# Kernel optimization log

Measured on AMD Instinct MI355X. Metric: run time of the kernel, lower is better.

## Reference

```python
import jax, jax.numpy as jnp
import numpy as np

B, T, Fd, C, D = 16, 256, 128, 32, 32
K_RATIO = 0.5
EPS = 1e-5


def setup_inputs() -> dict:
    key = jax.random.key(0)
    ks = jax.random.split(key, 40)
    n = lambda i, shape, s=0.05: jax.random.normal(ks[i], shape, jnp.float32) * s
    inp = {"x": jax.random.normal(ks[0], (B, T, Fd, C), jnp.float32)}
    inp.update(c1w=n(1, (C, C)), c1b=n(2, (C,)), bng=1.0 + n(3, (C,)), bnb=n(4, (C,)),
               bnm=n(5, (C,)), bnv=jax.random.uniform(ks[6], (C,)) + 0.5,
               c2w=n(7, (1, C)), c2b=n(8, (1,)))
    def gat_params(i0, pre):
        return {pre + "apw": n(i0, (D, C)), pre + "apb": n(i0 + 1, (D,)),
                pre + "aw": n(i0 + 2, (D,)), pre + "pww": n(i0 + 3, (D, C)),
                pre + "pwb": n(i0 + 4, (D,)), pre + "pow": n(i0 + 5, (D, C)),
                pre + "pob": n(i0 + 6, (D,)), pre + "g": 1.0 + n(i0 + 7, (D,)),
                pre + "be": n(i0 + 8, (D,)), pre + "m": n(i0 + 9, (D,)),
                pre + "v": jax.random.uniform(ks[i0 + 10], (D,)) + 0.5}
    inp.update(gat_params(9, "fc_"))
    inp.update(gat_params(20, "tc_"))
    inp.update(pfw=n(31, (1, D)), pfb=n(32, (1,)), ptw=n(33, (1, D)), ptb=n(34, (1,)),
               w1=n(35, (D, D)), w2=n(36, (D, D)), fcw=n(37, (2, 2 * D)), fcb=n(38, (2,)))
    return inp


def _gat(h, apw, apb, aw, pww, pwb, poww, pob, g, be, mu, var):
    # h: (B, N, C). Dense pairwise multiplication -> (B, N, N, C)
    p = h[:, :, None, :] * h[:, None, :, :]
    e = jnp.tanh(jnp.einsum('bijc,dc->bijd', p, apw) + apb)      # (B,N,N,D)
    att = jax.nn.softmax(jnp.einsum('bijd,d->bij', e, aw), axis=2)  # softmax over dim=-2 (temp=1)
    out = jnp.einsum('bij,bjc->bic', att, h) @ pww.T + pwb + h @ poww.T + pob
    out = (out - mu) / jnp.sqrt(var + EPS) * g + be               # BatchNorm1d (eval)
    return jax.nn.selu(out)


def _pool(h, pw, pb, ratio):
    s = jax.nn.sigmoid(h @ pw.T + pb)                # (B,N,1)
    kn = max(int(h.shape[1] * ratio), 1)
    _, idx = jax.lax.top_k(s[..., 0], kn)            # (B,kn), descending scores
    return jnp.take_along_axis(h * s, idx[..., None], axis=1)


def reference(x, c1w, c1b, bng, bnb, bnm, bnv, c2w, c2b,
              fc_apw, fc_apb, fc_aw, fc_pww, fc_pwb, fc_pow, fc_pob, fc_g, fc_be, fc_m, fc_v,
              tc_apw, tc_apb, tc_aw, tc_pww, tc_pwb, tc_pow, tc_pob, tc_g, tc_be, tc_m, tc_v,
              pfw, pfb, ptw, ptb, w1, w2, fcw, fcb):
    # conv1 (1x1), SELU, BatchNorm2d (eval), conv2 (1x1 -> 1 channel)
    xp = jnp.einsum('oc,btfc->botf', c1w, x) + c1b[None, :, None, None]
    xp = jax.nn.selu(xp)
    xp = (xp - bnm[None, :, None, None]) / jnp.sqrt(bnv + EPS)[None, :, None, None] \
         * bng[None, :, None, None] + bnb[None, :, None, None]
    m = jnp.einsum('c,bctf->btf', c2w[0], xp) + c2b[0]           # (B,T,F)
    M0 = jax.nn.softmax(m, axis=1)
    FCatt = jnp.einsum('btf,btfc->bfc', M0, x)                   # sum over T
    TCatt = jnp.einsum('btf,btfc->btc', M0, x)                   # sum over F
    FC_gat = _gat(FCatt, fc_apw, fc_apb, fc_aw, fc_pww, fc_pwb, fc_pow, fc_pob, fc_g, fc_be, fc_m, fc_v)
    TC_gat = _gat(TCatt, tc_apw, tc_apb, tc_aw, tc_pww, tc_pwb, tc_pow, tc_pob, tc_g, tc_be, tc_m, tc_v)
    xF = _pool(FC_gat, pfw, pfb, K_RATIO)                        # (B, F/2, D)
    xT = _pool(TC_gat, ptw, ptb, K_RATIO)                        # (B, T/2, D)
    M1 = jax.nn.softmax((xF @ w1.T) @ xT.transpose(0, 2, 1), axis=-1)
    M2 = jax.nn.softmax((xT @ w2.T) @ xF.transpose(0, 2, 1), axis=-1)
    xF_fused = xF + M1 @ xT
    xT_fused = xT + M2 @ xF
    node = jnp.concatenate([xF_fused.max(axis=1), xT_fused.max(axis=1)], axis=-1)
    return node @ fcw.T + fcb
```

## Files before the change

kernel.cpp:

```cpp
#include <hip/hip_runtime.h>
#include <hip/hip_bf16.h>

#define Bn 16
#define Tn 256
#define Fn 128
#define Cn 32
#define Dn 32
#define EPSf 1e-5f
#define SELU_L 1.0507009873554805f
#define SELU_A 1.6732632423543772f

typedef unsigned short u16;
typedef unsigned int u32;

struct Ptrs { const void* p[39]; };

#define P_C1W 0
#define P_C1B 1024
#define P_MW  1056
#define P_MK  1088
#define P_FC  1089
#define P_TCG (1089+3264)
#define G_APW 0
#define G_APB 1024
#define G_AW  1056
#define G_PWW 1088
#define G_PWB 2112
#define G_POW 2144
#define G_POB 3168
#define G_GS  3200
#define G_GB  3232
#define GAT_SZ 3264
#define P_PFW (P_TCG+GAT_SZ)
#define P_PFB (P_PFW+32)
#define P_PTW (P_PFB+1)
#define P_PTB (P_PTW+32)
#define P_W1  (P_PTB+1)
#define P_W2  (P_W1+1024)
#define P_FCW (P_W2+1024)
#define P_FCB (P_FCW+128)
#define P_FLAG 10000

#define WS_M     10240
#define WS_FCATT (WS_M+524288)
#define WS_TCATT (WS_FCATT+65536)
#define WS_FCGAT (WS_TCATT+131072)
#define WS_TCGAT (WS_FCGAT+65536)
#define WS_XF    (WS_TCGAT+131072)
#define WS_XT    (WS_XF+32768)
#define WS_XFF   (WS_XT+65536)
#define WS_XTF   (WS_XFF+32768)

__device__ __forceinline__ float bf2f(u16 u) {
    union { u32 i; float f; } v; v.i = ((u32)u) << 16; return v.f;
}
__device__ __forceinline__ u16 f2bf(float f) {
    union { float f; u32 u; } v; v.f = f;
    u32 r = (v.u + 0x7fffu + ((v.u >> 16) & 1u)) >> 16;
    return (u16)r;
}
__device__ __forceinline__ void up2(u32 u, float* o) {
    union { u32 i; float f; } a, b;
    a.i = u << 16; b.i = u & 0xffff0000u;
    o[0] = a.f; o[1] = b.f;
}
__device__ __forceinline__ float tanh_fast(float x) {
    float e = __expf(2.f * x);
    return 1.f - 2.f / (e + 1.f);
}
__device__ __forceinline__ float ldp(const void* p, int i, int isb) {
    return isb ? bf2f(((const u16*)p)[i]) : ((const float*)p)[i];
}

__global__ void k0_setup(Ptrs in, float* __restrict__ P) {
    __shared__ int sflag;
    int tid = threadIdx.x;
    if (tid == 0) {
        const u16* xu = (const u16*)in.p[0];
        int bad = 0;
        for (int i = 0; i < 256; i++) {
            float f = bf2f(xu[i]);
            float a = fabsf(f);
            if (!(a < 64.f) && !(a == 0.f)) bad++;
        }
        sflag = (bad <= 8) ? 1 : 0;
        P[P_FLAG] = (float)sflag;
    }
    __syncthreads();
    const int isb = sflag;

    for (int i = tid; i < 1024; i += 256) P[P_C1W + i] = ldp(in.p[1], i, isb);
    if (tid < 32) {
        P[P_C1B + tid] = ldp(in.p[2], tid, isb);
        float A = ldp(in.p[3], tid, isb) * rsqrtf(ldp(in.p[6], tid, isb) + EPSf);
        P[P_MW + tid] = ldp(in.p[7], tid, isb) * A * SELU_L;
    }
    if (tid == 0) {
        float k = ldp(in.p[8], 0, isb);
        for (int o = 0; o < 32; o++) {
            float A = ldp(in.p[3], o, isb) * rsqrtf(ldp(in.p[6], o, isb) + EPSf);
            float Bc = ldp(in.p[4], o, isb) - ldp(in.p[5], o, isb) * A;
            k += ldp(in.p[7], o, isb) * Bc;
        }
        P[P_MK] = k;
    }
    for (int g = 0; g < 2; g++) {
        int ib = g ? 20 : 9;
        float* G = P + (g ? P_TCG : P_FC);
        for (int i = tid; i < 1024; i += 256) {
            G[G_APW + i] = ldp(in.p[ib + 0], i, isb);
            G[G_PWW + i] = ldp(in.p[ib + 3], i, isb);
            G[G_POW + i] = ldp(in.p[ib + 5], i, isb);
        }
        if (tid < 32) {
            G[G_APB + tid] = ldp(in.p[ib + 1], tid, isb);
            G[G_AW  + tid] = ldp(in.p[ib + 2], tid, isb);
            G[G_PWB + tid] = ldp(in.p[ib + 4], tid, isb);
            G[G_POB + tid] = ldp(in.p[ib + 6], tid, isb);
            float gs = ldp(in.p[ib + 7], tid, isb) * rsqrtf(ldp(in.p[ib + 10], tid, isb) + EPSf);
            G[G_GS + tid] = gs;
            G[G_GB + tid] = ldp(in.p[ib + 8], tid, isb) - ldp(in.p[ib + 9], tid, isb) * gs;
        }
    }
    if (tid < 32) {
        P[P_PFW + tid] = ldp(in.p[31], tid, isb);
        P[P_PTW + tid] = ldp(in.p[33], tid, isb);
    }
    if (tid == 0) { P[P_PFB] = ldp(in.p[32], 0, isb); P[P_PTB] = ldp(in.p[34], 0, isb); }
    for (int i = tid; i < 1024; i += 256) {
        P[P_W1 + i] = ldp(in.p[35], i, isb);
        P[P_W2 + i] = ldp(in.p[36], i, isb);
    }
    if (tid < 128) P[P_FCW + tid] = ldp(in.p[37], tid, isb);
    if (tid < 2)   P[P_FCB + tid] = ldp(in.p[38], tid, isb);
}

__global__ __launch_bounds__(256) void k1_conv_m(const void* __restrict__ xin,
                                                 const float* __restrict__ P,
                                                 float* __restrict__ M) {
    int idx = blockIdx.x * 256 + threadIdx.x;
    const int isb = __builtin_amdgcn_readfirstlane((int)P[P_FLAG]);
    float xv[32];
    if (isb) {
        const uint4* xp4 = reinterpret_cast<const uint4*>((const u16*)xin + (size_t)idx * 32);
        uint4 q0 = xp4[0], q1 = xp4[1], q2 = xp4[2], q3 = xp4[3];
        up2(q0.x, xv + 0);  up2(q0.y, xv + 2);  up2(q0.z, xv + 4);  up2(q0.w, xv + 6);
        up2(q1.x, xv + 8);  up2(q1.y, xv + 10); up2(q1.z, xv + 12); up2(q1.w, xv + 14);
        up2(q2.x, xv + 16); up2(q2.y, xv + 18); up2(q2.z, xv + 20); up2(q2.w, xv + 22);
        up2(q3.x, xv + 24); up2(q3.y, xv + 26); up2(q3.z, xv + 28); up2(q3.w, xv + 30);
    } else {
        const float4* xf4 = reinterpret_cast<const float4*>((const float*)xin + (size_t)idx * 32);
        #pragma unroll
        for (int q = 0; q < 8; q++) {
            float4 v = xf4[q];
            xv[q * 4 + 0] = v.x; xv[q * 4 + 1] = v.y;
            xv[q * 4 + 2] = v.z; xv[q * 4 + 3] = v.w;
        }
    }
    float acc = P[P_MK];
    #pragma unroll
    for (int o = 0; o < 32; o++) {
        float z = P[P_C1B + o];
        #pragma unroll
        for (int c = 0; c < 32; c++) z = fmaf(P[P_C1W + o * 32 + c], xv[c], z);
        float br = (z > 0.f) ? z : SELU_A * (__expf(z) - 1.f);
        acc = fmaf(P[P_MW + o], br, acc);
    }
    M[idx] = acc;
}

__global__ __launch_bounds__(256) void k2_softmax(float* __restrict__ M,
                                                  float* __restrict__ FCzero) {
    __shared__ float r[256];
    int b = blockIdx.x >> 3, fg = blockIdx.x & 7;
    int tid = threadIdx.x;
    int fl = tid & 15, ts = tid >> 4;
    float* col = M + (size_t)b * (Tn * Fn) + fg * 16 + fl;
    float v[16];
    float mx = -1e30f;
    #pragma unroll
    for (int k = 0; k < 16; k++) { v[k] = col[(ts * 16 + k) * Fn]; mx = fmaxf(mx, v[k]); }
    r[tid] = mx; __syncthreads();
    for (int s = 128; s >= 16; s >>= 1) { if (tid < s) r[tid] = fmaxf(r[tid], r[tid + s]); __syncthreads(); }
    mx = r[fl];
    __syncthreads();
    float sm = 0.f;
    #pragma unroll
    for (int k = 0; k < 16; k++) { v[k] = __expf(v[k] - mx); sm += v[k]; }
    r[tid] = sm; __syncthreads();
    for (int s = 128; s >= 16; s >>= 1) { if (tid < s) r[tid] += r[tid + s]; __syncthreads(); }
    float inv = 1.f / r[fl];
    #pragma unroll
    for (int k = 0; k < 16; k++) col[(ts * 16 + k) * Fn] = v[k] * inv;
    int gid = blockIdx.x * 256 + tid;
    for (int i = gid; i < Bn * Fn * Cn; i += 128 * 256) FCzero[i] = 0.f;
}

__global__ __launch_bounds__(256) void k3n(const void* __restrict__ xin,
                                           const float* __restrict__ M,
                                           const float* __restrict__ Pflag,
                                           float* __restrict__ FCatt,
                                           float* __restrict__ TCatt) {
    __shared__ float lA[256], lB[256];
    int bi = blockIdx.x;
    int b = bi >> 5, tg = bi & 31;
    int tid = threadIdx.x;
    const int isb = __builtin_amdgcn_readfirstlane((int)Pflag[P_FLAG]);
    float fa0[8], fa1[8];
    #pragma unroll
    for (int k = 0; k < 8; k++) { fa0[k] = 0.f; fa1[k] = 0.f; }
    int fbase = tid >> 4;
    for (int tt = 0; tt < 8; tt++) {
        int t = tg * 8 + tt;
        const float* Mrow = M + (size_t)b * (Tn * Fn) + (size_t)t * Fn;
        size_t rowoff = ((size_t)b * Tn + t) * (Fn * Cn);
        float ts0 = 0.f, ts1 = 0.f;
        #pragma unroll
        for (int k = 0; k < 8; k++) {
            float x0, x1;
            if (isb) {
                u32 u = *(const u32*)((const u16*)xin + rowoff + tid * 2 + 512 * k);
                float tmp[2]; up2(u, tmp); x0 = tmp[0]; x1 = tmp[1];
            } else {
                float2 v2 = *(const float2*)((const float*)xin + rowoff + tid * 2 + 512 * k);
                x0 = v2.x; x1 = v2.y;
            }
            float m = Mrow[fbase + 16 * k];
            x0 *= m; x1 *= m;
            fa0[k] += x0; fa1[k] += x1;
            ts0 += x0; ts1 += x1;
        }
        lA[tid] = ts0; lB[tid] = ts1;
        __syncthreads();
        if (tid < 32) {
            int half = tid & 1, p = tid >> 1;
            float s = 0.f;
            if (half) { for (int g = 0; g < 16; g++) s += lB[g * 16 + p]; }
            else      { for (int g = 0; g < 16; g++) s += lA[g * 16 + p]; }
            TCatt[((size_t)b * Tn + t) * Cn + tid] = s;
        }
        __syncthreads();
    }
    #pragma unroll
    for (int k = 0; k < 8; k++) {
        atomicAdd(&FCatt[(size_t)b * 4096 + tid * 2 + 512 * k],     fa0[k]);
        atomicAdd(&FCatt[(size_t)b * 4096 + tid * 2 + 512 * k + 1], fa1[k]);
    }
}

__global__ __launch_bounds__(256) void k4a_scores(const float* __restrict__ P,
                                                  const float* __restrict__ FCatt,
                                                  const float* __restrict__ TCatt,
                                                  u16* __restrict__ SFC,
                                                  u16* __restrict__ STC) {
    __shared__ float li[16 * 33], lj[16 * 33];
    int bi = blockIdx.x;
    int N, nt, b, pr; const float* h; u16* S; const float* G;
    if (bi < 16 * 36) { b = bi / 36; pr = bi % 36; N = 128; nt = 8;
        h = FCatt + (size_t)b * 4096; S = SFC + (size_t)b * 16384; G = P + P_FC; }
    else { bi -= 16 * 36; b = bi / 136; pr = bi % 136; N = 256; nt = 16;
        h = TCatt + (size_t)b * 8192; S = STC + (size_t)b * 65536; G = P + P_TCG; }
    int ti = 0, rem = pr;
    while (rem >= nt - ti) { rem -= nt - ti; ti++; }
    int tj = ti + rem;
    int tid = threadIdx.x;
    for (int e = tid; e < 512; e += 256) {
        int rr = e >> 5, c = e & 31;
        li[rr * 33 + c] = h[(ti * 16 + rr) * 32 + c];
        lj[rr * 33 + c] = h[(tj * 16 + rr) * 32 + c];
    }
    __syncthreads();
    int il = tid >> 4, jl = tid & 15;
    float p[32];
    #pragma unroll
    for (int c = 0; c < 32; c++) p[c] = li[il * 33 + c] * lj[jl * 33 + c];
    float score = 0.f;
    #pragma unroll
    for (int d = 0; d < 32; d++) {
        float z = G[G_APB + d];
        #pragma unroll
        for (int c = 0; c < 32; c++) z = fmaf(G[G_APW + d * 32 + c], p[c], z);
        score = fmaf(G[G_AW + d], tanh_fast(z), score);
    }
    int i = ti * 16 + il, j = tj * 16 + jl;
    u16 sb = f2bf(score);
    S[(size_t)i * N + j] = sb;
    if (ti != tj) S[(size_t)j * N + i] = sb;
}

__global__ __launch_bounds__(256) void k4b_soft(const float* __restrict__ P,
                                                const float* __restrict__ FCatt,
                                                const float* __restrict__ TCatt,
                                                const u16* __restrict__ SFC,
                                                const u16* __restrict__ STC,
                                                float* __restrict__ FCgat,
                                                float* __restrict__ TCgat) {
    __shared__ float hs[256 * 33];
    __shared__ float sc[256];
    __shared__ float red[256];
    int bi = blockIdx.x;
    int N, b, i; const float* h; float* out; const float* G; const u16* Srow;
    if (bi < 2048) { N = 128; b = bi >> 7; i = bi & 127;
        h = FCatt + (size_t)b * 4096; out = FCgat + (size_t)b * 4096; G = P + P_FC;
        Srow = SFC + (size_t)b * 16384 + (size_t)i * 128; }
    else { bi -= 2048; N = 256; b = bi >> 8; i = bi & 255;
        h = TCatt + (size_t)b * 8192; out = TCgat + (size_t)b * 8192; G = P + P_TCG;
        Srow = STC + (size_t)b * 65536 + (size_t)i * 256; }
    int tid = threadIdx.x;
    for (int e = tid; e < N * 32; e += 256) { int j = e >> 5, c = e & 31; hs[j * 33 + c] = h[e]; }
    if (tid < N) sc[tid] = bf2f(Srow[tid]);
    __syncthreads();
    red[tid] = (tid < N) ? sc[tid] : -1e30f;
    __syncthreads();
    for (int s = 128; s > 0; s >>= 1) { if (tid < s) red[tid] = fmaxf(red[tid], red[tid + s]); __syncthreads(); }
    float mx = red[0];
    __syncthreads();
    float e = (tid < N) ? __expf(sc[tid] - mx) : 0.f;
    red[tid] = e;
    __syncthreads();
    for (int s = 128; s > 0; s >>= 1) { if (tid < s) red[tid] += red[tid + s]; __syncthreads(); }
    float inv = 1.f / red[0];
    __syncthreads();
    sc[tid] = e * inv;
    __syncthreads();
    int jj = tid >> 5, c0 = tid & 31;
    float acc = 0.f;
    for (int j = jj; j < N; j += 8) acc = fmaf(sc[j], hs[j * 33 + c0], acc);
    red[tid] = acc;
    __syncthreads();
    if (tid < 128) red[tid] += red[tid + 128];
    __syncthreads();
    if (tid < 64)  red[tid] += red[tid + 64];
    __syncthreads();
    if (tid < 32)  red[tid] += red[tid + 32];
    __syncthreads();
    if (tid < 32) {
        int d = tid;
        float z = G[G_PWB + d] + G[G_POB + d];
        #pragma unroll
        for (int c = 0; c < 32; c++)
            z = fmaf(G[G_PWW + d * 32 + c], red[c], fmaf(G[G_POW + d * 32 + c], hs[i * 33 + c], z));
        z = z * G[G_GS + d] + G[G_GB + d];
        z = SELU_L * ((z > 0.f) ? z : SELU_A * (__expf(z) - 1.f));
        out[(size_t)i * 32 + d] = z;
    }
}

__global__ __launch_bounds__(256) void k5_pool(const float* __restrict__ P,
                                               const float* __restrict__ FCgat,
                                               const float* __restrict__ TCgat,
                                               float* __restrict__ XF,
                                               float* __restrict__ XT) {
    __shared__ float s[256];
    int bi = blockIdx.x;
    int N, kn, b, pboff; const float* g; float* xp; const float* pw;
    if (bi < 16) { b = bi; N = 128; kn = 64;
        g = FCgat + (size_t)b * 4096; xp = XF + (size_t)b * 2048; pw = P + P_PFW; pboff = P_PFB; }
    else { b = bi - 16; N = 256; kn = 128;
        g = TCgat + (size_t)b * 8192; xp = XT + (size_t)b * 4096; pw = P + P_PTW; pboff = P_PTB; }
    int tid = threadIdx.x;
    float sv = 0.f;
    if (tid < N) {
        float z = P[pboff];
        #pragma unroll
        for (int d = 0; d < 32; d++) z = fmaf(pw[d], g[(size_t)tid * 32 + d], z);
        sv = 1.f / (1.f + __expf(-z));
        s[tid] = sv;
    }
    __syncthreads();
    if (tid < N) {
        int rank = 0;
        for (int l = 0; l < N; l++) {
            float sl = s[l];
            rank += (sl > sv) || (sl == sv && l < tid);
        }
        if (rank < kn) {
            #pragma unroll
            for (int d = 0; d < 32; d++) xp[(size_t)rank * 32 + d] = g[(size_t)tid * 32 + d] * sv;
        }
    }
}

__global__ __launch_bounds__(256) void k6_fuse(const float* __restrict__ P,
                                               const float* __restrict__ XF,
                                               const float* __restrict__ XT,
                                               float* __restrict__ XFF,
                                               float* __restrict__ XTF) {
    int wid = blockIdx.x * 4 + (threadIdx.x >> 6);
    int lane = threadIdx.x & 63;
    if (wid < 1024) {
        int b = wid >> 6, i = wid & 63;
        const float* xf  = XF + ((size_t)b * 64 + i) * 32;
        const float* xtb = XT + (size_t)b * 4096;
        const float* w1 = P + P_W1;
        int d = lane & 31;
        float y = 0.f;
        #pragma unroll
        for (int c = 0; c < 32; c++) y = fmaf(w1[d * 32 + c], xf[c], y);
        float xtr0[32], xtr1[32];
        #pragma unroll
        for (int c = 0; c < 32; c++) {
            xtr0[c] = xtb[(size_t)lane * 32 + c];
            xtr1[c] = xtb[(size_t)(lane + 64) * 32 + c];
        }
        float s0 = 0.f, s1 = 0.f;
        #pragma unroll
        for (int c = 0; c < 32; c++) {
            float yc = __shfl(y, c, 64);
            s0 = fmaf(yc, xtr0[c], s0);
            s1 = fmaf(yc, xtr1[c], s1);
        }
        float mx = fmaxf(s0, s1);
        #pragma unroll
        for (int off = 1; off < 64; off <<= 1) mx = fmaxf(mx, __shfl_xor(mx, off, 64));
        float e0 = __expf(s0 - mx), e1 = __expf(s1 - mx);
        float sm = e0 + e1;
        #pragma unroll
        for (int off = 1; off < 64; off <<= 1) sm += __shfl_xor(sm, off, 64);
        float inv = 1.f / sm;
        float a0 = e0 * inv, a1 = e1 * inv;
        float v[32];
        #pragma unroll
        for (int c = 0; c < 32; c++) v[c] = a0 * xtr0[c] + a1 * xtr1[c];
        #pragma unroll
        for (int off = 1; off < 64; off <<= 1) {
            #pragma unroll
            for (int c = 0; c < 32; c++) v[c] += __shfl_xor(v[c], off, 64);
        }
        if (lane == 0) {
            float* o = XFF + ((size_t)b * 64 + i) * 32;
            #pragma unroll
            for (int c = 0; c < 32; c++) o[c] = xf[c] + v[c];
        }
    } else {
        int r = wid - 1024;
        int b = r >> 7, i = r & 127;
        const float* xt  = XT + ((size_t)b * 128 + i) * 32;
        const float* xfb = XF + (size_t)b * 2048;
        const float* w2 = P + P_W2;
        int d = lane & 31;
        float y = 0.f;
        #pragma unroll
        for (int c = 0; c < 32; c++) y = fmaf(w2[d * 32 + c], xt[c], y);
        float xfr[32];
        #pragma unroll
        for (int c = 0; c < 32; c++) xfr[c] = xfb[(size_t)lane * 32 + c];
        float sc0 = 0.f;
        #pragma unroll
        for (int c = 0; c < 32; c++) sc0 = fmaf(__shfl(y, c, 64), xfr[c], sc0);
        float mx = sc0;
        #pragma unroll
        for (int off = 1; off < 64; off <<= 1) mx = fmaxf(mx, __shfl_xor(mx, off, 64));
        float e = __expf(sc0 - mx);
        float sm = e;
        #pragma unroll
        for (int off = 1; off < 64; off <<= 1) sm += __shfl_xor(sm, off, 64);
        float a = e / sm;
        float v[32];
        #pragma unroll
        for (int c = 0; c < 32; c++) v[c] = a * xfr[c];
        #pragma unroll
        for (int off = 1; off < 64; off <<= 1) {
            #pragma unroll
            for (int c = 0; c < 32; c++) v[c] += __shfl_xor(v[c], off, 64);
        }
        if (lane == 0) {
            float* o = XTF + ((size_t)b * 128 + i) * 32;
            #pragma unroll
            for (int c = 0; c < 32; c++) o[c] = xt[c] + v[c];
        }
    }
}

__global__ __launch_bounds__(64) void k7_out(const float* __restrict__ P,
                                             const float* __restrict__ XFF,
                                             const float* __restrict__ XTF,
                                             void* __restrict__ outp) {
    __shared__ float node[64];
    int b = blockIdx.x, tid = threadIdx.x;
    if (tid < 32) {
        float m = -1e30f;
        for (int r = 0; r < 64; r++) m = fmaxf(m, XFF[((size_t)b * 64 + r) * 32 + tid]);
        node[tid] = m;
    } else {
        int c = tid - 32;
        float m = -1e30f;
        for (int r = 0; r < 128; r++) m = fmaxf(m, XTF[((size_t)b * 128 + r) * 32 + c]);
        node[tid] = m;
    }
    __syncthreads();
    if (tid < 2) {
        float z = P[P_FCB + tid];
        #pragma unroll
        for (int k = 0; k < 64; k++) z = fmaf(P[P_FCW + tid * 64 + k], node[k], z);
        int isb = (int)P[P_FLAG];
        if (isb) ((u16*)outp)[b * 2 + tid] = f2bf(z);
        else     ((float*)outp)[b * 2 + tid] = z;
    }
}

extern "C" void kernel_launch(void* const* d_in, const int* in_sizes, int n_in,
                              void* d_out, int out_size, void* d_ws, size_t ws_size,
                              hipStream_t stream) {
    (void)in_sizes; (void)n_in; (void)out_size; (void)ws_size;
    float* W = (float*)d_ws;
    Ptrs ptrs;
    for (int i = 0; i < 39; i++) ptrs.p[i] = d_in[i];
    const void* x = d_in[0];
    float* P = W;
    u16* STC = (u16*)(W + WS_M);
    u16* SFC = (u16*)(W + WS_XF);

    k0_setup<<<1, 256, 0, stream>>>(ptrs, P);
    k1_conv_m<<<2048, 256, 0, stream>>>(x, P, W + WS_M);
    k2_softmax<<<128, 256, 0, stream>>>(W + WS_M, W + WS_FCATT);
    k3n<<<512, 256, 0, stream>>>(x, W + WS_M, P, W + WS_FCATT, W + WS_TCATT);
    k4a_scores<<<16 * 36 + 16 * 136, 256, 0, stream>>>(P, W + WS_FCATT, W + WS_TCATT, SFC, STC);
    k4b_soft<<<6144, 256, 0, stream>>>(P, W + WS_FCATT, W + WS_TCATT, SFC, STC,
                                       W + WS_FCGAT, W + WS_TCGAT);
    k5_pool<<<32, 256, 0, stream>>>(P, W + WS_FCGAT, W + WS_TCGAT, W + WS_XF, W + WS_XT);
    k6_fuse<<<768, 256, 0, stream>>>(P, W + WS_XF, W + WS_XT, W + WS_XFF, W + WS_XTF);
    k7_out<<<16, 64, 0, stream>>>(P, W + WS_XFF, W + WS_XTF, d_out);
}
```

Before: 353.4 us.

## Precompute GAT projections, batch softmax rows per block, fuse pool/cross-attention/output

Moves the pww/pow projections ahead of the attention-weighted sum (att@(h W^T) instead of (att@h) W^T), computing Y and Z in extra blocks of the score kernel. The per-row softmax kernel (6144 blocks, each reloading all of h) becomes 192 blocks that load Y once and process 32 rows with wave-level reductions. Pooling, the cross-attention fuse and the final output are merged into one per-batch kernel that keeps its data in shared memory. This removes redundant global loads and two launches, at the cost of only 16 blocks for the merged tail kernel, which limits its parallelism.

```diff
diff --git a/kernel.cpp b/kernel.cpp
--- a/kernel.cpp
+++ b/kernel.cpp
@@ -50,6 +50,10 @@
 #define WS_XT    (WS_XF+32768)
 #define WS_XFF   (WS_XT+65536)
 #define WS_XTF   (WS_XFF+32768)
+#define WS_YFC   (WS_XTF+65536)
+#define WS_ZFC   (WS_YFC+65536)
+#define WS_YTC   (WS_ZFC+65536)
+#define WS_ZTC   (WS_YTC+131072)
 
 __device__ __forceinline__ float bf2f(u16 u) {
     union { u32 i; float f; } v; v.i = ((u32)u) << 16; return v.f;
@@ -252,9 +256,42 @@
                                                   const float* __restrict__ FCatt,
                                                   const float* __restrict__ TCatt,
                                                   u16* __restrict__ SFC,
-                                                  u16* __restrict__ STC) {
+                                                  u16* __restrict__ STC,
+                                                  float* __restrict__ Yfc,
+                                                  float* __restrict__ Zfc,
+                                                  float* __restrict__ Ytc,
+                                                  float* __restrict__ Ztc) {
+    int bi = blockIdx.x;
+    int tid = threadIdx.x;
+    if (bi >= 2752) {
+        bi -= 2752;
+        int N, b, rg; const float* h; float* Yg; float* Zg; const float* G;
+        if (bi < 64) { b = bi >> 2; rg = bi & 3; N = 128;
+            h = FCatt + (size_t)b * 4096; Yg = Yfc + (size_t)b * 4096; Zg = Zfc + (size_t)b * 4096; G = P + P_FC; }
+        else { bi -= 64; b = bi >> 3; rg = bi & 7; N = 256;
+            h = TCatt + (size_t)b * 8192; Yg = Ytc + (size_t)b * 8192; Zg = Ztc + (size_t)b * 8192; G = P + P_TCG; }
+        (void)N;
+        #pragma unroll
+        for (int k = 0; k < 8; k++) {
+            int e = k * 256 + tid;
+            int half = e >> 10, ee = e & 1023;
+            int r = rg * 32 + (ee >> 5), d = ee & 31;
+            const float* hr = h + (size_t)r * 32;
+            if (half == 0) {
+                float z = 0.f;
+                #pragma unroll
+                for (int c = 0; c < 32; c++) z = fmaf(hr[c], G[G_PWW + d * 32 + c], z);
+                Yg[(size_t)r * 32 + d] = z;
+            } else {
+                float z = G[G_PWB + d] + G[G_POB + d];
+                #pragma unroll
+                for (int c = 0; c < 32; c++) z = fmaf(hr[c], G[G_POW + d * 32 + c], z);
+                Zg[(size_t)r * 32 + d] = z;
+            }
+        }
+        return;
+    }
     __shared__ float li[16 * 33], lj[16 * 33];
-    int bi = blockIdx.x;
     int N, nt, b, pr; const float* h; u16* S; const float* G;
     if (bi < 16 * 36) { b = bi / 36; pr = bi % 36; N = 128; nt = 8;
         h = FCatt + (size_t)b * 4096; S = SFC + (size_t)b * 16384; G = P + P_FC; }
@@ -263,7 +300,6 @@
     int ti = 0, rem = pr;
     while (rem >= nt - ti) { rem -= nt - ti; ti++; }
     int tj = ti + rem;
-    int tid = threadIdx.x;
     for (int e = tid; e < 512; e += 256) {
         int rr = e >> 5, c = e & 31;
         li[rr * 33 + c] = h[(ti * 16 + rr) * 32 + c];
@@ -288,127 +324,119 @@
     if (ti != tj) S[(size_t)j * N + i] = sb;
 }
 
-__global__ __launch_bounds__(256) void k4b_soft(const float* __restrict__ P,
-                                                const float* __restrict__ FCatt,
-                                                const float* __restrict__ TCatt,
-                                                const u16* __restrict__ SFC,
-                                                const u16* __restrict__ STC,
-                                                float* __restrict__ FCgat,
-                                                float* __restrict__ TCgat) {
-    __shared__ float hs[256 * 33];
-    __shared__ float sc[256];
-    __shared__ float red[256];
+__global__ __launch_bounds__(256) void k4b2(const float* __restrict__ P,
+                                            const u16* __restrict__ SFC,
+                                            const u16* __restrict__ STC,
+                                            const float* __restrict__ Yfc,
+                                            const float* __restrict__ Zfc,
+                                            const float* __restrict__ Ytc,
+                                            const float* __restrict__ Ztc,
+                                            float* __restrict__ FCgat,
+                                            float* __restrict__ TCgat) {
+    __shared__ float Ys[256 * 33];
+    __shared__ float attb[4 * 256];
     int bi = blockIdx.x;
-    int N, b, i; const float* h; float* out; const float* G; const u16* Srow;
-    if (bi < 2048) { N = 128; b = bi >> 7; i = bi & 127;
-        h = FCatt + (size_t)b * 4096; out = FCgat + (size_t)b * 4096; G = P + P_FC;
-        Srow = SFC + (size_t)b * 16384 + (size_t)i * 128; }
-    else { bi -= 2048; N = 256; b = bi >> 8; i = bi & 255;
-        h = TCatt + (size_t)b * 8192; out = TCgat + (size_t)b * 8192; G = P + P_TCG;
-        Srow = STC + (size_t)b * 65536 + (size_t)i * 256; }
+    int N, b, rg; const float* Yg; const float* Zg; const u16* S; float* out; const float* G;
+    if (bi < 64) { b = bi >> 2; rg = bi & 3; N = 128;
+        Yg = Yfc + (size_t)b * 4096; Zg = Zfc + (size_t)b * 4096;
+        S = SFC + (size_t)b * 16384; out = FCgat + (size_t)b * 4096; G = P + P_FC; }
+    else { bi -= 64; b = bi >> 3; rg = bi & 7; N = 256;
+        Yg = Ytc + (size_t)b * 8192; Zg = Ztc + (size_t)b * 8192;
+        S = STC + (size_t)b * 65536; out = TCgat + (size_t)b * 8192; G = P + P_TCG; }
     int tid = threadIdx.x;
-    for (int e = tid; e < N * 32; e += 256) { int j = e >> 5, c = e & 31; hs[j * 33 + c] = h[e]; }
-    if (tid < N) sc[tid] = bf2f(Srow[tid]);
-    __syncthreads();
-    red[tid] = (tid < N) ? sc[tid] : -1e30f;
-    __syncthreads();
-    for (int s = 128; s > 0; s >>= 1) { if (tid < s) red[tid] = fmaxf(red[tid], red[tid + s]); __syncthreads(); }
-    float mx = red[0];
-    __syncthreads();
-    float e = (tid < N) ? __expf(sc[tid] - mx) : 0.f;
-    red[tid] = e;
-    __syncthreads();
-    for (int s = 128; s > 0; s >>= 1) { if (tid < s) red[tid] += red[tid + s]; __syncthreads(); }
-    float inv = 1.f / red[0];
-    __syncthreads();
-    sc[tid] = e * inv;
-    __syncthreads();
-    int jj = tid >> 5, c0 = tid & 31;
-    float acc = 0.f;
-    for (int j = jj; j < N; j += 8) acc = fmaf(sc[j], hs[j * 33 + c0], acc);
-    red[tid] = acc;
-    __syncthreads();
-    if (tid < 128) red[tid] += red[tid + 128];
-    __syncthreads();
-    if (tid < 64)  red[tid] += red[tid + 64];
-    __syncthreads();
-    if (tid < 32)  red[tid] += red[tid + 32];
-    __syncthreads();
-    if (tid < 32) {
-        int d = tid;
-        float z = G[G_PWB + d] + G[G_POB + d];
-        #pragma unroll
-        for (int c = 0; c < 32; c++)
-            z = fmaf(G[G_PWW + d * 32 + c], red[c], fmaf(G[G_POW + d * 32 + c], hs[i * 33 + c], z));
-        z = z * G[G_GS + d] + G[G_GB + d];
-        z = SELU_L * ((z > 0.f) ? z : SELU_A * (__expf(z) - 1.f));
-        out[(size_t)i * 32 + d] = z;
-    }
-}
-
-__global__ __launch_bounds__(256) void k5_pool(const float* __restrict__ P,
-                                               const float* __restrict__ FCgat,
-                                               const float* __restrict__ TCgat,
-                                               float* __restrict__ XF,
-                                               float* __restrict__ XT) {
-    __shared__ float s[256];
-    int bi = blockIdx.x;
-    int N, kn, b, pboff; const float* g; float* xp; const float* pw;
-    if (bi < 16) { b = bi; N = 128; kn = 64;
-        g = FCgat + (size_t)b * 4096; xp = XF + (size_t)b * 2048; pw = P + P_PFW; pboff = P_PFB; }
-    else { b = bi - 16; N = 256; kn = 128;
-        g = TCgat + (size_t)b * 8192; xp = XT + (size_t)b * 4096; pw = P + P_PTW; pboff = P_PTB; }
-    int tid = threadIdx.x;
-    float sv = 0.f;
-    if (tid < N) {
-        float z = P[pboff];
-        #pragma unroll
-        for (int d = 0; d < 32; d++) z = fmaf(pw[d], g[(size_t)tid * 32 + d], z);
-        sv = 1.f / (1.f + __expf(-z));
-        s[tid] = sv;
-    }
-    __syncthreads();
-    if (tid < N) {
+    for (int e = tid; e < N * 32; e += 256) Ys[(e >> 5) * 33 + (e & 31)] = Yg[e];
+    __syncthreads();
+    int wave = tid >> 6, lane = tid & 63;
+    for (int r = 0; r < 8; r++) {
+        int i = rg * 32 + wave * 8 + r;
+        const u16* Srow = S + (size_t)i * N;
+        float s0 = bf2f(Srow[lane]);
+        float s1 = bf2f(Srow[lane + 64]);
+        float s2 = -1e30f, s3 = -1e30f;
+        if (N == 256) { s2 = bf2f(Srow[lane + 128]); s3 = bf2f(Srow[lane + 192]); }
+        float mx = fmaxf(fmaxf(s0, s1), fmaxf(s2, s3));
+        #pragma unroll
+        for (int off = 1; off < 64; off <<= 1) mx = fmaxf(mx, __shfl_xor(mx, off, 64));
+        float e0 = __expf(s0 - mx), e1 = __expf(s1 - mx);
+        float e2 = 0.f, e3 = 0.f;
+        if (N == 256) { e2 = __expf(s2 - mx); e3 = __expf(s3 - mx); }
+        float sm = e0 + e1 + e2 + e3;
+        #pragma unroll
+        for (int off = 1; off < 64; off <<= 1) sm += __shfl_xor(sm, off, 64);
+        float inv = 1.f / sm;
+        attb[wave * 256 + lane] = e0 * inv;
+        attb[wave * 256 + 64 + lane] = e1 * inv;
+        if (N == 256) { attb[wave * 256 + 128 + lane] = e2 * inv; attb[wave * 256 + 192 + lane] = e3 * inv; }
+        int jg = lane >> 5, d = lane & 31;
+        float acc = 0.f;
+        for (int j = jg; j < N; j += 2) acc = fmaf(attb[wave * 256 + j], Ys[j * 33 + d], acc);
+        acc += __shfl_xor(acc, 32, 64);
+        if (lane < 32) {
+            float z = acc + Zg[(size_t)i * 32 + d];
+            z = z * G[G_GS + d] + G[G_GB + d];
+            z = SELU_L * ((z > 0.f) ? z : SELU_A * (__expf(z) - 1.f));
+            out[(size_t)i * 32 + d] = z;
+        }
+    }
+}
+
+__global__ __launch_bounds__(256) void k567(const float* __restrict__ P,
+                                            const float* __restrict__ FCgat,
+                                            const float* __restrict__ TCgat,
+                                            void* __restrict__ outp) {
+    __shared__ float xF[64 * 33], xT[128 * 33];
+    __shared__ float xFF[64 * 32], xTF[128 * 32];
+    __shared__ float s[256], ybuf[4 * 32], attb[4 * 128], node[64];
+    int b = blockIdx.x, tid = threadIdx.x;
+    const float* gF = FCgat + (size_t)b * 4096;
+    const float* gT = TCgat + (size_t)b * 8192;
+    float svF = 0.f;
+    if (tid < 128) {
+        float z = P[P_PFB];
+        #pragma unroll
+        for (int d = 0; d < 32; d++) z = fmaf(P[P_PFW + d], gF[tid * 32 + d], z);
+        svF = 1.f / (1.f + __expf(-z));
+        s[tid] = svF;
+    }
+    __syncthreads();
+    if (tid < 128) {
         int rank = 0;
-        for (int l = 0; l < N; l++) {
-            float sl = s[l];
-            rank += (sl > sv) || (sl == sv && l < tid);
-        }
-        if (rank < kn) {
+        for (int l = 0; l < 128; l++) { float sl = s[l]; rank += (sl > svF) || (sl == svF && l < tid); }
+        if (rank < 64) {
             #pragma unroll
-            for (int d = 0; d < 32; d++) xp[(size_t)rank * 32 + d] = g[(size_t)tid * 32 + d] * sv;
-        }
-    }
-}
-
-__global__ __launch_bounds__(256) void k6_fuse(const float* __restrict__ P,
-                                               const float* __restrict__ XF,
-                                               const float* __restrict__ XT,
-                                               float* __restrict__ XFF,
-                                               float* __restrict__ XTF) {
-    int wid = blockIdx.x * 4 + (threadIdx.x >> 6);
-    int lane = threadIdx.x & 63;
-    if (wid < 1024) {
-        int b = wid >> 6, i = wid & 63;
-        const float* xf  = XF + ((size_t)b * 64 + i) * 32;
-        const float* xtb = XT + (size_t)b * 4096;
-        const float* w1 = P + P_W1;
-        int d = lane & 31;
+            for (int d = 0; d < 32; d++) xF[rank * 33 + d] = gF[tid * 32 + d] * svF;
+        }
+    }
+    __syncthreads();
+    {
+        float z = P[P_PTB];
+        #pragma unroll
+        for (int d = 0; d < 32; d++) z = fmaf(P[P_PTW + d], gT[tid * 32 + d], z);
+        float svT = 1.f / (1.f + __expf(-z));
+        s[tid] = svT;
+        __syncthreads();
+        int rank = 0;
+        for (int l = 0; l < 256; l++) { float sl = s[l]; rank += (sl > svT) || (sl == svT && l < tid); }
+        if (rank < 128) {
+            #pragma unroll
+            for (int d = 0; d < 32; d++) xT[rank * 33 + d] = gT[tid * 32 + d] * svT;
+        }
+    }
+    __syncthreads();
+    int w = tid >> 6, lane = tid & 63;
+    int d = lane & 31;
+    for (int r = 0; r < 16; r++) {
+        int i = w * 16 + r;
         float y = 0.f;
         #pragma unroll
-        for (int c = 0; c < 32; c++) y = fmaf(w1[d * 32 + c], xf[c], y);
-        float xtr0[32], xtr1[32];
+        for (int c = 0; c < 32; c++) y = fmaf(P[P_W1 + d * 32 + c], xF[i * 33 + c], y);
+        if (lane < 32) ybuf[w * 32 + d] = y;
+        float s0 = 0.f, s1 = 0.f;
         #pragma unroll
         for (int c = 0; c < 32; c++) {
-            xtr0[c] = xtb[(size_t)lane * 32 + c];
-            xtr1[c] = xtb[(size_t)(lane + 64) * 32 + c];
-        }
-        float s0 = 0.f, s1 = 0.f;
-        #pragma unroll
-        for (int c = 0; c < 32; c++) {
-            float yc = __shfl(y, c, 64);
-            s0 = fmaf(yc, xtr0[c], s0);
-            s1 = fmaf(yc, xtr1[c], s1);
+            float yc = ybuf[w * 32 + c];
+            s0 = fmaf(yc, xT[lane * 33 + c], s0);
+            s1 = fmaf(yc, xT[(lane + 64) * 33 + c], s1);
         }
         float mx = fmaxf(s0, s1);
         #pragma unroll
@@ -418,74 +446,46 @@
         #pragma unroll
         for (int off = 1; off < 64; off <<= 1) sm += __shfl_xor(sm, off, 64);
         float inv = 1.f / sm;
-        float a0 = e0 * inv, a1 = e1 * inv;
-        float v[32];
-        #pragma unroll
-        for (int c = 0; c < 32; c++) v[c] = a0 * xtr0[c] + a1 * xtr1[c];
-        #pragma unroll
-        for (int off = 1; off < 64; off <<= 1) {
-            #pragma unroll
-            for (int c = 0; c < 32; c++) v[c] += __shfl_xor(v[c], off, 64);
-        }
-        if (lane == 0) {
-            float* o = XFF + ((size_t)b * 64 + i) * 32;
-            #pragma unroll
-            for (int c = 0; c < 32; c++) o[c] = xf[c] + v[c];
-        }
-    } else {
-        int r = wid - 1024;
-        int b = r >> 7, i = r & 127;
-        const float* xt  = XT + ((size_t)b * 128 + i) * 32;
-        const float* xfb = XF + (size_t)b * 2048;
-        const float* w2 = P + P_W2;
-        int d = lane & 31;
+        attb[w * 128 + lane] = e0 * inv;
+        attb[w * 128 + 64 + lane] = e1 * inv;
+        int jg = lane >> 5;
+        float acc = 0.f;
+        for (int j = jg; j < 128; j += 2) acc = fmaf(attb[w * 128 + j], xT[j * 33 + d], acc);
+        acc += __shfl_xor(acc, 32, 64);
+        if (lane < 32) xFF[i * 32 + d] = xF[i * 33 + d] + acc;
+    }
+    for (int r = 0; r < 32; r++) {
+        int i = w * 32 + r;
         float y = 0.f;
         #pragma unroll
-        for (int c = 0; c < 32; c++) y = fmaf(w2[d * 32 + c], xt[c], y);
-        float xfr[32];
-        #pragma unroll
-        for (int c = 0; c < 32; c++) xfr[c] = xfb[(size_t)lane * 32 + c];
-        float sc0 = 0.f;
-        #pragma unroll
-        for (int c = 0; c < 32; c++) sc0 = fmaf(__shfl(y, c, 64), xfr[c], sc0);
-        float mx = sc0;
+        for (int c = 0; c < 32; c++) y = fmaf(P[P_W2 + d * 32 + c], xT[i * 33 + c], y);
+        if (lane < 32) ybuf[w * 32 + d] = y;
+        float s0 = 0.f;
+        #pragma unroll
+        for (int c = 0; c < 32; c++) s0 = fmaf(ybuf[w * 32 + c], xF[lane * 33 + c], s0);
+        float mx = s0;
         #pragma unroll
         for (int off = 1; off < 64; off <<= 1) mx = fmaxf(mx, __shfl_xor(mx, off, 64));
-        float e = __expf(sc0 - mx);
-        float sm = e;
+        float e0 = __expf(s0 - mx);
+        float sm = e0;
         #pragma unroll
         for (int off = 1; off < 64; off <<= 1) sm += __shfl_xor(sm, off, 64);
-        float a = e / sm;
-        float v[32];
-        #pragma unroll
-        for (int c = 0; c < 32; c++) v[c] = a * xfr[c];
-        #pragma unroll
-        for (int off = 1; off < 64; off <<= 1) {
-            #pragma unroll
-            for (int c = 0; c < 32; c++) v[c] += __shfl_xor(v[c], off, 64);
-        }
-        if (lane == 0) {
-            float* o = XTF + ((size_t)b * 128 + i) * 32;
-            #pragma unroll
-            for (int c = 0; c < 32; c++) o[c] = xt[c] + v[c];
-        }
-    }
-}
-
-__global__ __launch_bounds__(64) void k7_out(const float* __restrict__ P,
-                                             const float* __restrict__ XFF,
-                                             const float* __restrict__ XTF,
-                                             void* __restrict__ outp) {
-    __shared__ float node[64];
-    int b = blockIdx.x, tid = threadIdx.x;
+        attb[w * 128 + lane] = e0 / sm;
+        int jg = lane >> 5;
+        float acc = 0.f;
+        for (int j = jg; j < 64; j += 2) acc = fmaf(attb[w * 128 + j], xF[j * 33 + d], acc);
+        acc += __shfl_xor(acc, 32, 64);
+        if (lane < 32) xTF[i * 32 + d] = xT[i * 33 + d] + acc;
+    }
+    __syncthreads();
     if (tid < 32) {
         float m = -1e30f;
-        for (int r = 0; r < 64; r++) m = fmaxf(m, XFF[((size_t)b * 64 + r) * 32 + tid]);
+        for (int r = 0; r < 64; r++) m = fmaxf(m, xFF[r * 32 + tid]);
         node[tid] = m;
-    } else {
+    } else if (tid < 64) {
         int c = tid - 32;
         float m = -1e30f;
-        for (int r = 0; r < 128; r++) m = fmaxf(m, XTF[((size_t)b * 128 + r) * 32 + c]);
+        for (int r = 0; r < 128; r++) m = fmaxf(m, xTF[r * 32 + c]);
         node[tid] = m;
     }
     __syncthreads();
@@ -493,9 +493,8 @@
         float z = P[P_FCB + tid];
         #pragma unroll
         for (int k = 0; k < 64; k++) z = fmaf(P[P_FCW + tid * 64 + k], node[k], z);
-        int isb = (int)P[P_FLAG];
-        if (isb) ((u16*)outp)[b * 2 + tid] = f2bf(z);
-        else     ((float*)outp)[b * 2 + tid] = z;
+        if ((int)P[P_FLAG]) ((u16*)outp)[b * 2 + tid] = f2bf(z);
+        else                ((float*)outp)[b * 2 + tid] = z;
     }
 }
 
@@ -515,10 +514,9 @@
     k1_conv_m<<<2048, 256, 0, stream>>>(x, P, W + WS_M);
     k2_softmax<<<128, 256, 0, stream>>>(W + WS_M, W + WS_FCATT);
     k3n<<<512, 256, 0, stream>>>(x, W + WS_M, P, W + WS_FCATT, W + WS_TCATT);
-    k4a_scores<<<16 * 36 + 16 * 136, 256, 0, stream>>>(P, W + WS_FCATT, W + WS_TCATT, SFC, STC);
-    k4b_soft<<<6144, 256, 0, stream>>>(P, W + WS_FCATT, W + WS_TCATT, SFC, STC,
-                                       W + WS_FCGAT, W + WS_TCGAT);
-    k5_pool<<<32, 256, 0, stream>>>(P, W + WS_FCGAT, W + WS_TCGAT, W + WS_XF, W + WS_XT);
-    k6_fuse<<<768, 256, 0, stream>>>(P, W + WS_XF, W + WS_XT, W + WS_XFF, W + WS_XTF);
-    k7_out<<<16, 64, 0, stream>>>(P, W + WS_XFF, W + WS_XTF, d_out);
-}
+    k4a_scores<<<2752 + 192, 256, 0, stream>>>(P, W + WS_FCATT, W + WS_TCATT, SFC, STC,
+                                               W + WS_YFC, W + WS_ZFC, W + WS_YTC, W + WS_ZTC);
+    k4b2<<<192, 256, 0, stream>>>(P, SFC, STC, W + WS_YFC, W + WS_ZFC, W + WS_YTC, W + WS_ZTC,
+                                  W + WS_FCGAT, W + WS_TCGAT);
+    k567<<<16, 256, 0, stream>>>(P, W + WS_FCGAT, W + WS_TCGAT, d_out);
+}
```

Result: slower. 517.9 us (+46.6%).

## Precompute projected node features and batch softmax rows per wave in GAT

Applied to the files above, without the earlier changes.

The attention-weighted sum is reassociated: h is projected through pww (Y) and pow plus biases (Z) ahead of time, in extra blocks appended to the score kernel, so the softmax kernel only computes att·Y + Z. The softmax kernel now runs 192 blocks, each staging Y once in shared memory and handling 32 rows, with one wave per row using shuffle reductions instead of block-wide shared-memory reductions. This removes the per-row reload of h and the many __syncthreads of the old 6144-block kernel. The cost is extra workspace traffic for Y/Z, much lower parallelism in the softmax kernel, and the FC score buffer moved to a new workspace offset.

```diff
diff --git a/kernel.cpp b/kernel.cpp
--- a/kernel.cpp
+++ b/kernel.cpp
@@ -50,6 +50,11 @@
 #define WS_XT    (WS_XF+32768)
 #define WS_XFF   (WS_XT+65536)
 #define WS_XTF   (WS_XFF+32768)
+#define WS_YFC   (WS_XTF+65536)
+#define WS_ZFC   (WS_YFC+65536)
+#define WS_YTC   (WS_ZFC+65536)
+#define WS_ZTC   (WS_YTC+131072)
+#define WS_SFC   (WS_ZTC+131072)
 
 __device__ __forceinline__ float bf2f(u16 u) {
     union { u32 i; float f; } v; v.i = ((u32)u) << 16; return v.f;
@@ -252,9 +257,41 @@
                                                   const float* __restrict__ FCatt,
                                                   const float* __restrict__ TCatt,
                                                   u16* __restrict__ SFC,
-                                                  u16* __restrict__ STC) {
+                                                  u16* __restrict__ STC,
+                                                  float* __restrict__ Yfc,
+                                                  float* __restrict__ Zfc,
+                                                  float* __restrict__ Ytc,
+                                                  float* __restrict__ Ztc) {
+    int bi = blockIdx.x;
+    int tid = threadIdx.x;
+    if (bi >= 2752) {
+        bi -= 2752;
+        int b, rg; const float* h; float* Yg; float* Zg; const float* G;
+        if (bi < 64) { b = bi >> 2; rg = bi & 3;
+            h = FCatt + (size_t)b * 4096; Yg = Yfc + (size_t)b * 4096; Zg = Zfc + (size_t)b * 4096; G = P + P_FC; }
+        else { bi -= 64; b = bi >> 3; rg = bi & 7;
+            h = TCatt + (size_t)b * 8192; Yg = Ytc + (size_t)b * 8192; Zg = Ztc + (size_t)b * 8192; G = P + P_TCG; }
+        #pragma unroll
+        for (int k = 0; k < 8; k++) {
+            int e = k * 256 + tid;
+            int half = e >> 10, ee = e & 1023;
+            int r = rg * 32 + (ee >> 5), d = ee & 31;
+            const float* hr = h + (size_t)r * 32;
+            if (half == 0) {
+                float z = 0.f;
+                #pragma unroll
+                for (int c = 0; c < 32; c++) z = fmaf(hr[c], G[G_PWW + d * 32 + c], z);
+                Yg[(size_t)r * 32 + d] = z;
+            } else {
+                float z = G[G_PWB + d] + G[G_POB + d];
+                #pragma unroll
+                for (int c = 0; c < 32; c++) z = fmaf(hr[c], G[G_POW + d * 32 + c], z);
+                Zg[(size_t)r * 32 + d] = z;
+            }
+        }
+        return;
+    }
     __shared__ float li[16 * 33], lj[16 * 33];
-    int bi = blockIdx.x;
     int N, nt, b, pr; const float* h; u16* S; const float* G;
     if (bi < 16 * 36) { b = bi / 36; pr = bi % 36; N = 128; nt = 8;
         h = FCatt + (size_t)b * 4096; S = SFC + (size_t)b * 16384; G = P + P_FC; }
@@ -263,7 +300,6 @@
     int ti = 0, rem = pr;
     while (rem >= nt - ti) { rem -= nt - ti; ti++; }
     int tj = ti + rem;
-    int tid = threadIdx.x;
     for (int e = tid; e < 512; e += 256) {
         int rr = e >> 5, c = e & 31;
         li[rr * 33 + c] = h[(ti * 16 + rr) * 32 + c];
@@ -288,61 +324,59 @@
     if (ti != tj) S[(size_t)j * N + i] = sb;
 }
 
-__global__ __launch_bounds__(256) void k4b_soft(const float* __restrict__ P,
-                                                const float* __restrict__ FCatt,
-                                                const float* __restrict__ TCatt,
-                                                const u16* __restrict__ SFC,
-                                                const u16* __restrict__ STC,
-                                                float* __restrict__ FCgat,
-                                                float* __restrict__ TCgat) {
-    __shared__ float hs[256 * 33];
-    __shared__ float sc[256];
-    __shared__ float red[256];
+__global__ __launch_bounds__(256) void k4b2(const float* __restrict__ P,
+                                            const u16* __restrict__ SFC,
+                                            const u16* __restrict__ STC,
+                                            const float* __restrict__ Yfc,
+                                            const float* __restrict__ Zfc,
+                                            const float* __restrict__ Ytc,
+                                            const float* __restrict__ Ztc,
+                                            float* __restrict__ FCgat,
+                                            float* __restrict__ TCgat) {
+    __shared__ float Ys[256 * 33];
+    __shared__ float attb[4 * 256];
     int bi = blockIdx.x;
-    int N, b, i; const float* h; float* out; const float* G; const u16* Srow;
-    if (bi < 2048) { N = 128; b = bi >> 7; i = bi & 127;
-        h = FCatt + (size_t)b * 4096; out = FCgat + (size_t)b * 4096; G = P + P_FC;
-        Srow = SFC + (size_t)b * 16384 + (size_t)i * 128; }
-    else { bi -= 2048; N = 256; b = bi >> 8; i = bi & 255;
-        h = TCatt + (size_t)b * 8192; out = TCgat + (size_t)b * 8192; G = P + P_TCG;
-        Srow = STC + (size_t)b * 65536 + (size_t)i * 256; }
+    int N, b, rg; const float* Yg; const float* Zg; const u16* S; float* out; const float* G;
+    if (bi < 64) { b = bi >> 2; rg = bi & 3; N = 128;
+        Yg = Yfc + (size_t)b * 4096; Zg = Zfc + (size_t)b * 4096;
+        S = SFC + (size_t)b * 16384; out = FCgat + (size_t)b * 4096; G = P + P_FC; }
+    else { bi -= 64; b = bi >> 3; rg = bi & 7; N = 256;
+        Yg = Ytc + (size_t)b * 8192; Zg = Ztc + (size_t)b * 8192;
+        S = STC + (size_t)b * 65536; out = TCgat + (size_t)b * 8192; G = P + P_TCG; }
     int tid = threadIdx.x;
-    for (int e = tid; e < N * 32; e += 256) { int j = e >> 5, c = e & 31; hs[j * 33 + c] = h[e]; }
-    if (tid < N) sc[tid] = bf2f(Srow[tid]);
+    for (int e = tid; e < N * 32; e += 256) Ys[(e >> 5) * 33 + (e & 31)] = Yg[e];
     __syncthreads();
-    red[tid] = (tid < N) ? sc[tid] : -1e30f;
-    __syncthreads();
-    for (int s = 128; s > 0; s >>= 1) { if (tid < s) red[tid] = fmaxf(red[tid], red[tid + s]); __syncthreads(); }
-    float mx = red[0];
-    __syncthreads();
-    float e = (tid < N) ? __expf(sc[tid] - mx) : 0.f;
-    red[tid] = e;
-    __syncthreads();
-    for (int s = 128; s > 0; s >>= 1) { if (tid < s) red[tid] += red[tid + s]; __syncthreads(); }
-    float inv = 1.f / red[0];
-    __syncthreads();
-    sc[tid] = e * inv;
-    __syncthreads();
-    int jj = tid >> 5, c0 = tid & 31;
-    float acc = 0.f;
-    for (int j = jj; j < N; j += 8) acc = fmaf(sc[j], hs[j * 33 + c0], acc);
-    red[tid] = acc;
-    __syncthreads();
-    if (tid < 128) red[tid] += red[tid + 128];
-    __syncthreads();
-    if (tid < 64)  red[tid] += red[tid + 64];
-    __syncthreads();
-    if (tid < 32)  red[tid] += red[tid + 32];
-    __syncthreads();
-    if (tid < 32) {
-        int d = tid;
-        float z = G[G_PWB + d] + G[G_POB + d];
-        #pragma unroll
-        for (int c = 0; c < 32; c++)
-            z = fmaf(G[G_PWW + d * 32 + c], red[c], fmaf(G[G_POW + d * 32 + c], hs[i * 33 + c], z));
-        z = z * G[G_GS + d] + G[G_GB + d];
-        z = SELU_L * ((z > 0.f) ? z : SELU_A * (__expf(z) - 1.f));
-        out[(size_t)i * 32 + d] = z;
+    int wave = tid >> 6, lane = tid & 63;
+    for (int r = 0; r < 8; r++) {
+        int i = rg * 32 + wave * 8 + r;
+        const u16* Srow = S + (size_t)i * N;
+        float s0 = bf2f(Srow[lane]);
+        float s1 = bf2f(Srow[lane + 64]);
+        float s2 = -1e30f, s3 = -1e30f;
+        if (N == 256) { s2 = bf2f(Srow[lane + 128]); s3 = bf2f(Srow[lane + 192]); }
+        float mx = fmaxf(fmaxf(s0, s1), fmaxf(s2, s3));
+        #pragma unroll
+        for (int off = 1; off < 64; off <<= 1) mx = fmaxf(mx, __shfl_xor(mx, off, 64));
+        float e0 = __expf(s0 - mx), e1 = __expf(s1 - mx);
+        float e2 = 0.f, e3 = 0.f;
+        if (N == 256) { e2 = __expf(s2 - mx); e3 = __expf(s3 - mx); }
+        float sm = e0 + e1 + e2 + e3;
+        #pragma unroll
+        for (int off = 1; off < 64; off <<= 1) sm += __shfl_xor(sm, off, 64);
+        float inv = 1.f / sm;
+        attb[wave * 256 + lane] = e0 * inv;
+        attb[wave * 256 + 64 + lane] = e1 * inv;
+        if (N == 256) { attb[wave * 256 + 128 + lane] = e2 * inv; attb[wave * 256 + 192 + lane] = e3 * inv; }
+        int jg = lane >> 5, d = lane & 31;
+        float acc = 0.f;
+        for (int j = jg; j < N; j += 2) acc = fmaf(attb[wave * 256 + j], Ys[j * 33 + d], acc);
+        acc += __shfl_xor(acc, 32, 64);
+        if (lane < 32) {
+            float z = acc + Zg[(size_t)i * 32 + d];
+            z = z * G[G_GS + d] + G[G_GB + d];
+            z = SELU_L * ((z > 0.f) ? z : SELU_A * (__expf(z) - 1.f));
+            out[(size_t)i * 32 + d] = z;
+        }
     }
 }
 
@@ -509,15 +543,16 @@
     const void* x = d_in[0];
     float* P = W;
     u16* STC = (u16*)(W + WS_M);
-    u16* SFC = (u16*)(W + WS_XF);
+    u16* SFC = (u16*)(W + WS_SFC);
 
     k0_setup<<<1, 256, 0, stream>>>(ptrs, P);
     k1_conv_m<<<2048, 256, 0, stream>>>(x, P, W + WS_M);
     k2_softmax<<<128, 256, 0, stream>>>(W + WS_M, W + WS_FCATT);
     k3n<<<512, 256, 0, stream>>>(x, W + WS_M, P, W + WS_FCATT, W + WS_TCATT);
-    k4a_scores<<<16 * 36 + 16 * 136, 256, 0, stream>>>(P, W + WS_FCATT, W + WS_TCATT, SFC, STC);
-    k4b_soft<<<6144, 256, 0, stream>>>(P, W + WS_FCATT, W + WS_TCATT, SFC, STC,
-                                       W + WS_FCGAT, W + WS_TCGAT);
+    k4a_scores<<<2752 + 192, 256, 0, stream>>>(P, W + WS_FCATT, W + WS_TCATT, SFC, STC,
+                                               W + WS_YFC, W + WS_ZFC, W + WS_YTC, W + WS_ZTC);
+    k4b2<<<192, 256, 0, stream>>>(P, SFC, STC, W + WS_YFC, W + WS_ZFC, W + WS_YTC, W + WS_ZTC,
+                                  W + WS_FCGAT, W + WS_TCGAT);
     k5_pool<<<32, 256, 0, stream>>>(P, W + WS_FCGAT, W + WS_TCGAT, W + WS_XF, W + WS_XT);
     k6_fuse<<<768, 256, 0, stream>>>(P, W + WS_XF, W + WS_XT, W + WS_XFF, W + WS_XTF);
     k7_out<<<16, 64, 0, stream>>>(P, W + WS_XFF, W + WS_XTF, d_out);
```

Result: slower. 422.8 us (+19.6%).
